# Kernel tuning notes

Measured on AMD Instinct MI355X. Metric: run time of the kernel, lower is better.

## Reference

```python
import jax, jax.numpy as jnp
import numpy as np

B, S, D, H = 32, 256, 64, 512


def setup_inputs() -> dict:
    key = jax.random.key(0)
    ks = jax.random.split(key, 8)
    s = 1.0 / np.sqrt(H)
    u = lambda k, shp: jax.random.uniform(k, shp, jnp.float32, -s, s)
    return {
        "x": jax.random.normal(ks[0], (B, S, D), jnp.float32),
        "hidden_0": jax.random.normal(ks[1], (1, B, D), jnp.float32),
        "W_hid": u(ks[2], (H, D)),
        "b_hid": u(ks[3], (H,)),
        "W_ih": u(ks[4], (4 * H, S * D)),
        "W_hh": u(ks[5], (4 * H, H)),
        "b_ih": u(ks[6], (4 * H,)),
        "b_hh": u(ks[7], (4 * H,)),
    }


def reference(x, hidden_0, W_hid, b_hid, W_ih, W_hh, b_ih, b_hh):
    b, s, d = x.shape
    # h_0 = Linear(hidden_0): [1, B, H]; used as both h and c initial state
    h0 = hidden_0 @ W_hid.T + b_hid
    # growing triangular mask [S, S] (row i has i+1 ones)
    mask = jnp.tril(jnp.ones((s, s), x.dtype))
    # [B, S, S, D] -> [B, S, S*D]; row t of the LSTM input is x[:, :t+1] zero-padded
    newX = (mask[None, :, :, None] * x[:, None, :, :]).reshape(b, s, s * d)

    def step(carry, x_t):
        h, c = carry
        gates = x_t @ W_ih.T + h @ W_hh.T + (b_ih + b_hh)  # [B, 4H]
        i, f, g, o = jnp.split(gates, 4, axis=-1)  # torch gate order i,f,g,o
        i, f, o = jax.nn.sigmoid(i), jax.nn.sigmoid(f), jax.nn.sigmoid(o)
        g = jnp.tanh(g)
        c = f * c + i * g
        h = o * jnp.tanh(c)
        return (h, c), h

    _, hs = jax.lax.scan(step, (h0[0], h0[0]), newX.transpose(1, 0, 2))
    out = jax.nn.relu(hs.transpose(1, 0, 2))  # [B, S, H]
    return out, h0
```

## Files before the change

kernel.cpp:

```cpp
#include <hip/hip_runtime.h>
#include <math.h>

typedef __attribute__((ext_vector_type(8))) short short8;
typedef __attribute__((ext_vector_type(8))) _Float16 f16x8;
typedef __attribute__((ext_vector_type(4))) float f32x4;
typedef __attribute__((ext_vector_type(4))) unsigned uint32x4;

__device__ __forceinline__ void split_f16(float f, unsigned short& h, unsigned short& l){
  _Float16 hh = (_Float16)f;
  _Float16 ll = (_Float16)(f - (float)hh);
  h = __builtin_bit_cast(unsigned short, hh);
  l = __builtin_bit_cast(unsigned short, ll);
}

__device__ __forceinline__ float fsig(float xv){ return 1.f / (1.f + __expf(-xv)); }
__device__ __forceinline__ float ftanh(float xv){ return 1.f - 2.f / (1.f + __expf(2.f * xv)); }

__global__ __launch_bounds__(256, 1) void lstm_grp(
    const float* __restrict__ x,
    const float* __restrict__ hidden0,
    const float* __restrict__ W_hid,
    const float* __restrict__ b_hid,
    const float* __restrict__ W_ih,
    const float* __restrict__ W_hh,
    const float* __restrict__ b_ih,
    const float* __restrict__ b_hh,
    float* __restrict__ out,
    float* __restrict__ out_h0,
    unsigned* __restrict__ flags,
    unsigned short* __restrict__ hloc,
    unsigned short* __restrict__ hglb,
    unsigned short* __restrict__ xhi,
    unsigned short* __restrict__ xlo)
{
  __shared__ unsigned short hsb[2][16 * 64 * 8];

  const int tid  = threadIdx.x;
  const int bid  = blockIdx.x;
  const int grp  = bid & 7;
  const int slot = bid >> 3;
  const int lane = tid & 63;
  const int wid  = tid >> 6;
  const int m    = lane & 15;
  const int g    = lane >> 4;
  const int J0   = slot * 16;
  const int gid  = bid * 256 + tid;

  const int lbm   = m & 3;
  const int b_o   = grp * 4 + lbm;
  const int j_own = J0 + wid * 4 + g;
  const int R     = (m & 3) * 512 + J0 + wid * 4 + (m >> 2);
  const bool owner = (m < 4);

  unsigned short* hlg = hloc + (size_t)grp * 256 * 2048;
  unsigned short* hgg = hglb + (size_t)grp * 256 * 2048;

  {
    const float4* x4 = (const float4*)x;
    float4 f0 = x4[(size_t)gid * 2];
    float4 f1 = x4[(size_t)gid * 2 + 1];
    float fs[8] = {f0.x,f0.y,f0.z,f0.w,f1.x,f1.y,f1.z,f1.w};
    uint32x4 hv4, lv4;
    #pragma unroll
    for (int i = 0; i < 4; ++i){
      unsigned short h0b, l0b, h1b, l1b;
      split_f16(fs[2*i],   h0b, l0b);
      split_f16(fs[2*i+1], h1b, l1b);
      hv4[i] = (unsigned)h0b | ((unsigned)h1b << 16);
      lv4[i] = (unsigned)l0b | ((unsigned)l1b << 16);
    }
    asm volatile("global_store_dwordx4 %0, %1, off sc0 sc1" :: "v"(xhi + (size_t)gid*8), "v"(hv4) : "memory");
    asm volatile("global_store_dwordx4 %0, %1, off sc0 sc1" :: "v"(xlo + (size_t)gid*8), "v"(lv4) : "memory");
  }

  float c_state;
  {
    const float* hv = hidden0 + b_o * 64;
    const float* wv = W_hid + j_own * 64;
    float acc = b_hid[j_own];
    #pragma unroll
    for (int d = 0; d < 64; d += 4){
      float4 a = *(const float4*)(hv + d);
      float4 w = *(const float4*)(wv + d);
      acc += a.x*w.x + a.y*w.y + a.z*w.z + a.w*w.w;
    }
    c_state = acc;
    if (owner){
      out_h0[(size_t)b_o * 512 + j_own] = acc;
      unsigned short hh, ll; split_f16(acc, hh, ll);
      unsigned vh = hh;
      size_t off = (size_t)lbm * 512 + j_own;
      asm volatile("global_store_short %0, %1, off"         :: "v"(hlg + off), "v"(vh) : "memory");
      asm volatile("global_store_short %0, %1, off sc0 sc1" :: "v"(hgg + off), "v"(vh) : "memory");
    }
  }

  f16x8 whh_hi[16], whh_lo[16];
  #pragma unroll
  for (int kc = 0; kc < 16; ++kc){
    const float* p = W_hh + (size_t)R * 512 + kc * 32 + g * 8;
    float4 f0 = *(const float4*)p;
    float4 f1 = *(const float4*)(p + 4);
    float fs[8] = {f0.x,f0.y,f0.z,f0.w,f1.x,f1.y,f1.z,f1.w};
    short8 hb8, lb8;
    #pragma unroll
    for (int i = 0; i < 8; ++i){
      unsigned short hh, ll; split_f16(fs[i], hh, ll);
      hb8[i] = (short)hh; lb8[i] = (short)ll;
    }
    whh_hi[kc] = __builtin_bit_cast(f16x8, hb8);
    whh_lo[kc] = __builtin_bit_cast(f16x8, lb8);
  }

  const float bias_i = b_ih[j_own]        + b_hh[j_own];
  const float bias_f = b_ih[512 + j_own]  + b_hh[512 + j_own];
  const float bias_g = b_ih[1024 + j_own] + b_hh[1024 + j_own];
  const float bias_o = b_ih[1536 + j_own] + b_hh[1536 + j_own];

  asm volatile("s_waitcnt vmcnt(0)" ::: "memory");
  __syncthreads();
  if (tid == 0){
    unsigned one = 1;
    asm volatile("global_store_dword %0, %1, off sc0 sc1" :: "v"(flags + bid), "v"(one) : "memory");
  }
  {
    const unsigned* fp = flags + lane * 4;
    while (true){
      uint32x4 fv;
      asm volatile("global_load_dwordx4 %0, %1, off sc0 sc1\n\ts_waitcnt vmcnt(0)"
                   : "=v"(fv) : "v"(fp) : "memory");
      unsigned mn0 = fv[0] < fv[1] ? fv[0] : fv[1];
      unsigned mn1 = fv[2] < fv[3] ? fv[2] : fv[3];
      unsigned mn  = mn0 < mn1 ? mn0 : mn1;
      if (__all((int)(mn >= 1u))) break;
      __builtin_amdgcn_s_sleep(1);
    }
  }

  f32x4 axc0 = {0.f,0.f,0.f,0.f}, axc1 = axc0, axc2 = axc0;

  auto cvt8 = [](float4 f0, float4 f1, f16x8& hi, f16x8& lo){
    float fs[8] = {f0.x,f0.y,f0.z,f0.w,f1.x,f1.y,f1.z,f1.w};
    short8 hb8, lb8;
    #pragma unroll
    for (int i = 0; i < 8; ++i){
      unsigned short hh, ll; split_f16(fs[i], hh, ll);
      hb8[i] = (short)hh; lb8[i] = (short)ll;
    }
    hi = __builtin_bit_cast(f16x8, hb8);
    lo = __builtin_bit_cast(f16x8, lb8);
  };

  {
    #pragma unroll
    for (int kc = 0; kc < 2; ++kc){
      const float* p = W_ih + (size_t)R * 16384 + kc * 32 + g * 8;
      f16x8 ahi, alo;
      cvt8(*(const float4*)p, *(const float4*)(p + 4), ahi, alo);
      size_t off = (size_t)b_o * 16384 + kc * 32 + g * 8;
      f16x8 bhi = __builtin_bit_cast(f16x8, *(const short8*)(xhi + off));
      f16x8 blo = __builtin_bit_cast(f16x8, *(const short8*)(xlo + off));
      axc0 = __builtin_amdgcn_mfma_f32_16x16x32_f16(ahi, bhi, axc0, 0,0,0);
      axc1 = __builtin_amdgcn_mfma_f32_16x16x32_f16(ahi, blo, axc1, 0,0,0);
      axc2 = __builtin_amdgcn_mfma_f32_16x16x32_f16(alo, bhi, axc2, 0,0,0);
    }
  }

  const int lb_st = tid >> 6;
  const int us_st = (tid & 63) ^ (lb_st & 7);
  bool use_local = true;

  for (int t = 0; t < 256; ++t){
    uint32x4 dv;
    bool got = false;

    if (use_local){
      const unsigned* p = (const unsigned*)(hlg + (size_t)t * 2048) + (size_t)tid * 4;
      int tries = 0;
      while (tries < 64){
        asm volatile("global_load_dwordx4 %0, %1, off sc0\n\ts_waitcnt vmcnt(0)"
                     : "=v"(dv) : "v"(p) : "memory");
        int bad = 0;
        #pragma unroll
        for (int q = 0; q < 4; ++q){
          unsigned w = dv[q];
          bad |= ((w & 0xFFFFu) == 0xFFFFu) | (w >= 0xFFFF0000u);
        }
        if (!__any(bad)){ got = true; break; }
        __builtin_amdgcn_s_sleep(1);
        ++tries;
      }
      if (!got) use_local = false;
    }
    if (!got){
      const unsigned* p = (const unsigned*)(hgg + (size_t)t * 2048) + (size_t)tid * 4;
      while (true){
        asm volatile("global_load_dwordx4 %0, %1, off sc0 sc1\n\ts_waitcnt vmcnt(0)"
                     : "=v"(dv) : "v"(p) : "memory");
        int bad = 0;
        #pragma unroll
        for (int q = 0; q < 4; ++q){
          unsigned w = dv[q];
          bad |= ((w & 0xFFFFu) == 0xFFFFu) | (w >= 0xFFFF0000u);
        }
        if (!__any(bad)) break;
        __builtin_amdgcn_s_sleep(1);
      }
    }

    float4 w0, w1, w2, w3;
    short8 xh0, xh1, xl0, xl1;
    if (t < 255){
      const float* p = W_ih + (size_t)R * 16384 + (size_t)(t+1) * 64 + g * 8;
      w0 = *(const float4*)p;        w1 = *(const float4*)(p + 4);
      w2 = *(const float4*)(p + 32); w3 = *(const float4*)(p + 36);
      size_t off = ((size_t)b_o * 256 + (size_t)(t+1)) * 64 + g * 8;
      xh0 = *(const short8*)(xhi + off);      xh1 = *(const short8*)(xhi + off + 32);
      xl0 = *(const short8*)(xlo + off);      xl1 = *(const short8*)(xlo + off + 32);
    }

    *(uint32x4*)(&hsb[t & 1][(size_t)(lb_st * 64 + us_st) * 8]) = dv;
    __syncthreads();

    f32x4 acc0 = {0.f,0.f,0.f,0.f}, acc2 = acc0;
    {
      const unsigned short* srcH = &hsb[t & 1][0];
      #pragma unroll
      for (int kc = 0; kc < 16; ++kc){
        int us = (kc * 4 + g) ^ (m & 7);
        f16x8 bhi = __builtin_bit_cast(f16x8, *(const short8*)(srcH + (size_t)(m * 64 + us) * 8));
        acc0 = __builtin_amdgcn_mfma_f32_16x16x32_f16(whh_hi[kc], bhi, acc0, 0,0,0);
        acc2 = __builtin_amdgcn_mfma_f32_16x16x32_f16(whh_lo[kc], bhi, acc2, 0,0,0);
      }
    }

    f32x4 pre = acc0 + acc2 + axc0 + axc1 + axc2;
    float ig = fsig(pre[0] + bias_i);
    float fg = fsig(pre[1] + bias_f);
    float gg = ftanh(pre[2] + bias_g);
    float og = fsig(pre[3] + bias_o);
    c_state = fg * c_state + ig * gg;
    float hval = og * ftanh(c_state);

    if (owner){
      if (t < 255){
        unsigned short hh, ll; split_f16(hval, hh, ll);
        unsigned vh = hh;
        size_t off = (size_t)(t+1) * 2048 + (size_t)lbm * 512 + j_own;
        asm volatile("global_store_short %0, %1, off"         :: "v"(hlg + off), "v"(vh) : "memory");
        asm volatile("global_store_short %0, %1, off sc0 sc1" :: "v"(hgg + off), "v"(vh) : "memory");
      }
      out[((size_t)b_o * 256 + t) * 512 + j_own] = fmaxf(hval, 0.f);
    }

    if (t < 255){
      f16x8 ahi0, alo0, ahi1, alo1;
      cvt8(w0, w1, ahi0, alo0);
      cvt8(w2, w3, ahi1, alo1);
      f16x8 bh0 = __builtin_bit_cast(f16x8, xh0), bl0 = __builtin_bit_cast(f16x8, xl0);
      f16x8 bh1 = __builtin_bit_cast(f16x8, xh1), bl1 = __builtin_bit_cast(f16x8, xl1);
      axc0 = __builtin_amdgcn_mfma_f32_16x16x32_f16(ahi0, bh0, axc0, 0,0,0);
      axc1 = __builtin_amdgcn_mfma_f32_16x16x32_f16(ahi0, bl0, axc1, 0,0,0);
      axc2 = __builtin_amdgcn_mfma_f32_16x16x32_f16(alo0, bh0, axc2, 0,0,0);
      axc0 = __builtin_amdgcn_mfma_f32_16x16x32_f16(ahi1, bh1, axc0, 0,0,0);
      axc1 = __builtin_amdgcn_mfma_f32_16x16x32_f16(ahi1, bl1, axc1, 0,0,0);
      axc2 = __builtin_amdgcn_mfma_f32_16x16x32_f16(alo1, bh1, axc2, 0,0,0);
    }
  }
}

extern "C" void kernel_launch(void* const* d_in, const int* in_sizes, int n_in,
                              void* d_out, int out_size, void* d_ws, size_t ws_size,
                              hipStream_t stream) {
  const float* x       = (const float*)d_in[0];
  const float* hidden0 = (const float*)d_in[1];
  const float* W_hid   = (const float*)d_in[2];
  const float* b_hid   = (const float*)d_in[3];
  const float* W_ih    = (const float*)d_in[4];
  const float* W_hh    = (const float*)d_in[5];
  const float* b_ih    = (const float*)d_in[6];
  const float* b_hh    = (const float*)d_in[7];

  float* out    = (float*)d_out;
  float* out_h0 = out + (size_t)32 * 256 * 512;

  char* ws = (char*)d_ws;
  unsigned*       flags = (unsigned*)ws;
  unsigned short* xhi   = (unsigned short*)(ws + 4096);
  unsigned short* xlo   = (unsigned short*)(ws + 4096 + (1<<20));
  unsigned short* hloc  = (unsigned short*)(ws + 4096 + (2<<20));
  unsigned short* hglb  = (unsigned short*)(ws + 4096 + (2<<20) + (8<<20));

  (void)hipMemsetAsync(ws, 0, 4096, stream);
  (void)hipMemsetAsync(hloc, 0xFF, (size_t)8 * 256 * 2048 * 2, stream);
  (void)hipMemsetAsync(hglb, 0xFF, (size_t)8 * 256 * 2048 * 2, stream);

  lstm_grp<<<256, 256, 0, stream>>>(
      x, hidden0, W_hid, b_hid, W_ih, W_hh, b_ih, b_hh,
      out, out_h0, flags, hloc, hglb, xhi, xlo);
}
```

Measured before the change: 571.2 us.

## Precompute per-timestep input projections in fp32 prologue, prefix-sum them in the recurrence

Replaces the per-step split-fp16 MFMA computation of the input contribution with a prologue where each block computes, for one timestep chunk, the fp32 dot product of the 64-wide x slice with W_ih for all 2048 gate rows and 32 batches, storing the results to a workspace buffer. The recurrent loop then loads one prefetched 4-gate vector per step and accumulates it as a running prefix sum, exploiting the triangular mask structure. This moves W_ih reads and fp16 split conversions off the serial critical path. In exchange it adds a large fp32 scalar-FMA prologue reading all of W_ih (128 MB), plus a 64 MB workspace. The prologue writes must be visible to other blocks before the loop reads them, and that ordering relies on the existing flag barrier.

```diff
diff --git a/kernel.cpp b/kernel.cpp
--- a/kernel.cpp
+++ b/kernel.cpp
@@ -28,10 +28,9 @@
     float* __restrict__ out,
     float* __restrict__ out_h0,
     unsigned* __restrict__ flags,
+    float* __restrict__ Zb,
     unsigned short* __restrict__ hloc,
-    unsigned short* __restrict__ hglb,
-    unsigned short* __restrict__ xhi,
-    unsigned short* __restrict__ xlo)
+    unsigned short* __restrict__ hglb)
 {
   __shared__ unsigned short hsb[2][16 * 64 * 8];
 
@@ -44,7 +43,6 @@
   const int m    = lane & 15;
   const int g    = lane >> 4;
   const int J0   = slot * 16;
-  const int gid  = bid * 256 + tid;
 
   const int lbm   = m & 3;
   const int b_o   = grp * 4 + lbm;
@@ -56,21 +54,37 @@
   unsigned short* hgg = hglb + (size_t)grp * 256 * 2048;
 
   {
-    const float4* x4 = (const float4*)x;
-    float4 f0 = x4[(size_t)gid * 2];
-    float4 f1 = x4[(size_t)gid * 2 + 1];
-    float fs[8] = {f0.x,f0.y,f0.z,f0.w,f1.x,f1.y,f1.z,f1.w};
-    uint32x4 hv4, lv4;
+    const int tz = bid;
+    const int zb = tid & 31;
+    const int jq = tid >> 5;
+    float xrow[64];
+    const float* xp = x + ((size_t)zb * 256 + tz) * 64;
     #pragma unroll
-    for (int i = 0; i < 4; ++i){
-      unsigned short h0b, l0b, h1b, l1b;
-      split_f16(fs[2*i],   h0b, l0b);
-      split_f16(fs[2*i+1], h1b, l1b);
-      hv4[i] = (unsigned)h0b | ((unsigned)h1b << 16);
-      lv4[i] = (unsigned)l0b | ((unsigned)l1b << 16);
-    }
-    asm volatile("global_store_dwordx4 %0, %1, off sc0 sc1" :: "v"(xhi + (size_t)gid*8), "v"(hv4) : "memory");
-    asm volatile("global_store_dwordx4 %0, %1, off sc0 sc1" :: "v"(xlo + (size_t)gid*8), "v"(lv4) : "memory");
+    for (int d4 = 0; d4 < 16; ++d4){
+      float4 f = *(const float4*)(xp + d4 * 4);
+      xrow[d4*4+0] = f.x; xrow[d4*4+1] = f.y;
+      xrow[d4*4+2] = f.z; xrow[d4*4+3] = f.w;
+    }
+    for (int jj = 0; jj < 64; ++jj){
+      int j = jq * 64 + jj;
+      uint32x4 zw;
+      #pragma unroll
+      for (int gate = 0; gate < 4; ++gate){
+        const float* wp = W_ih + (size_t)(gate * 512 + j) * 16384 + (size_t)tz * 64;
+        float s0 = 0.f, s1 = 0.f, s2 = 0.f, s3 = 0.f;
+        #pragma unroll
+        for (int d4 = 0; d4 < 16; ++d4){
+          float4 w = *(const float4*)(wp + d4 * 4);
+          s0 += w.x * xrow[d4*4+0];
+          s1 += w.y * xrow[d4*4+1];
+          s2 += w.z * xrow[d4*4+2];
+          s3 += w.w * xrow[d4*4+3];
+        }
+        zw[gate] = __builtin_bit_cast(unsigned, (s0 + s1) + (s2 + s3));
+      }
+      float* zp = Zb + ((size_t)((size_t)tz * 512 + j) * 32 + zb) * 4;
+      asm volatile("global_store_dwordx4 %0, %1, off sc0 sc1" :: "v"(zp), "v"(zw) : "memory");
+    }
   }
 
   float c_state;
@@ -137,40 +151,18 @@
     }
   }
 
-  f32x4 axc0 = {0.f,0.f,0.f,0.f}, axc1 = axc0, axc2 = axc0;
-
-  auto cvt8 = [](float4 f0, float4 f1, f16x8& hi, f16x8& lo){
-    float fs[8] = {f0.x,f0.y,f0.z,f0.w,f1.x,f1.y,f1.z,f1.w};
-    short8 hb8, lb8;
-    #pragma unroll
-    for (int i = 0; i < 8; ++i){
-      unsigned short hh, ll; split_f16(fs[i], hh, ll);
-      hb8[i] = (short)hh; lb8[i] = (short)ll;
-    }
-    hi = __builtin_bit_cast(f16x8, hb8);
-    lo = __builtin_bit_cast(f16x8, lb8);
-  };
-
-  {
-    #pragma unroll
-    for (int kc = 0; kc < 2; ++kc){
-      const float* p = W_ih + (size_t)R * 16384 + kc * 32 + g * 8;
-      f16x8 ahi, alo;
-      cvt8(*(const float4*)p, *(const float4*)(p + 4), ahi, alo);
-      size_t off = (size_t)b_o * 16384 + kc * 32 + g * 8;
-      f16x8 bhi = __builtin_bit_cast(f16x8, *(const short8*)(xhi + off));
-      f16x8 blo = __builtin_bit_cast(f16x8, *(const short8*)(xlo + off));
-      axc0 = __builtin_amdgcn_mfma_f32_16x16x32_f16(ahi, bhi, axc0, 0,0,0);
-      axc1 = __builtin_amdgcn_mfma_f32_16x16x32_f16(ahi, blo, axc1, 0,0,0);
-      axc2 = __builtin_amdgcn_mfma_f32_16x16x32_f16(alo, bhi, axc2, 0,0,0);
-    }
-  }
-
   const int lb_st = tid >> 6;
   const int us_st = (tid & 63) ^ (lb_st & 7);
   bool use_local = true;
 
+  f32x4 axc = {0.f, 0.f, 0.f, 0.f};
+  f32x4 zc = *(const f32x4*)(Zb + ((size_t)((size_t)0 * 512 + j_own) * 32 + b_o) * 4);
+
   for (int t = 0; t < 256; ++t){
+    f32x4 zn;
+    if (t < 255)
+      zn = *(const f32x4*)(Zb + ((size_t)((size_t)(t+1) * 512 + j_own) * 32 + b_o) * 4);
+
     uint32x4 dv;
     bool got = false;
 
@@ -208,17 +200,6 @@
       }
     }
 
-    float4 w0, w1, w2, w3;
-    short8 xh0, xh1, xl0, xl1;
-    if (t < 255){
-      const float* p = W_ih + (size_t)R * 16384 + (size_t)(t+1) * 64 + g * 8;
-      w0 = *(const float4*)p;        w1 = *(const float4*)(p + 4);
-      w2 = *(const float4*)(p + 32); w3 = *(const float4*)(p + 36);
-      size_t off = ((size_t)b_o * 256 + (size_t)(t+1)) * 64 + g * 8;
-      xh0 = *(const short8*)(xhi + off);      xh1 = *(const short8*)(xhi + off + 32);
-      xl0 = *(const short8*)(xlo + off);      xl1 = *(const short8*)(xlo + off + 32);
-    }
-
     *(uint32x4*)(&hsb[t & 1][(size_t)(lb_st * 64 + us_st) * 8]) = dv;
     __syncthreads();
 
@@ -234,7 +215,9 @@
       }
     }
 
-    f32x4 pre = acc0 + acc2 + axc0 + axc1 + axc2;
+    axc += zc;
+
+    f32x4 pre = acc0 + acc2 + axc;
     float ig = fsig(pre[0] + bias_i);
     float fg = fsig(pre[1] + bias_f);
     float gg = ftanh(pre[2] + bias_g);
@@ -253,19 +236,7 @@
       out[((size_t)b_o * 256 + t) * 512 + j_own] = fmaxf(hval, 0.f);
     }
 
-    if (t < 255){
-      f16x8 ahi0, alo0, ahi1, alo1;
-      cvt8(w0, w1, ahi0, alo0);
-      cvt8(w2, w3, ahi1, alo1);
-      f16x8 bh0 = __builtin_bit_cast(f16x8, xh0), bl0 = __builtin_bit_cast(f16x8, xl0);
-      f16x8 bh1 = __builtin_bit_cast(f16x8, xh1), bl1 = __builtin_bit_cast(f16x8, xl1);
-      axc0 = __builtin_amdgcn_mfma_f32_16x16x32_f16(ahi0, bh0, axc0, 0,0,0);
-      axc1 = __builtin_amdgcn_mfma_f32_16x16x32_f16(ahi0, bl0, axc1, 0,0,0);
-      axc2 = __builtin_amdgcn_mfma_f32_16x16x32_f16(alo0, bh0, axc2, 0,0,0);
-      axc0 = __builtin_amdgcn_mfma_f32_16x16x32_f16(ahi1, bh1, axc0, 0,0,0);
-      axc1 = __builtin_amdgcn_mfma_f32_16x16x32_f16(ahi1, bl1, axc1, 0,0,0);
-      axc2 = __builtin_amdgcn_mfma_f32_16x16x32_f16(alo1, bh1, axc2, 0,0,0);
-    }
+    zc = zn;
   }
 }
 
@@ -286,10 +257,9 @@
 
   char* ws = (char*)d_ws;
   unsigned*       flags = (unsigned*)ws;
-  unsigned short* xhi   = (unsigned short*)(ws + 4096);
-  unsigned short* xlo   = (unsigned short*)(ws + 4096 + (1<<20));
-  unsigned short* hloc  = (unsigned short*)(ws + 4096 + (2<<20));
-  unsigned short* hglb  = (unsigned short*)(ws + 4096 + (2<<20) + (8<<20));
+  float*          Zb    = (float*)(ws + 4096);
+  unsigned short* hloc  = (unsigned short*)(ws + 4096 + (64u<<20));
+  unsigned short* hglb  = (unsigned short*)(ws + 4096 + (72u<<20));
 
   (void)hipMemsetAsync(ws, 0, 4096, stream);
   (void)hipMemsetAsync(hloc, 0xFF, (size_t)8 * 256 * 2048 * 2, stream);
@@ -297,5 +267,5 @@
 
   lstm_grp<<<256, 256, 0, stream>>>(
       x, hidden0, W_hid, b_hid, W_ih, W_hh, b_ih, b_hh,
-      out, out_h0, flags, hloc, hglb, xhi, xlo);
+      out, out_h0, flags, Zb, hloc, hglb);
 }
```

Result: slower. 743.7 us (+30.2%).

## Pack per-step hidden state in LDS and publish with vector stores

Applied to the files above, without the earlier changes.

Each block now gathers its 64 fp16 hidden values in shared memory and 8 threads write them with 16-byte stores to both the local and global exchange buffers. Previously every owner lane issued scattered 2-byte stores. The exchange buffer layout changes from batch-major to slot-major, and the LDS scatter indexing on the read side is updated to match. The output store moves after the input MFMA prefetch. The change aims to cut the number of coherent store transactions on the critical path between steps, at the cost of one extra block barrier per step.

```diff
diff --git a/kernel.cpp b/kernel.cpp
--- a/kernel.cpp
+++ b/kernel.cpp
@@ -34,6 +34,7 @@
     unsigned short* __restrict__ xlo)
 {
   __shared__ unsigned short hsb[2][16 * 64 * 8];
+  __shared__ unsigned short hpk[64];
 
   const int tid  = threadIdx.x;
   const int bid  = blockIdx.x;
@@ -88,10 +89,7 @@
     if (owner){
       out_h0[(size_t)b_o * 512 + j_own] = acc;
       unsigned short hh, ll; split_f16(acc, hh, ll);
-      unsigned vh = hh;
-      size_t off = (size_t)lbm * 512 + j_own;
-      asm volatile("global_store_short %0, %1, off"         :: "v"(hlg + off), "v"(vh) : "memory");
-      asm volatile("global_store_short %0, %1, off sc0 sc1" :: "v"(hgg + off), "v"(vh) : "memory");
+      hpk[m * 16 + wid * 4 + g] = hh;
     }
   }
 
@@ -117,6 +115,14 @@
   const float bias_g = b_ih[1024 + j_own] + b_hh[1024 + j_own];
   const float bias_o = b_ih[1536 + j_own] + b_hh[1536 + j_own];
 
+  __syncthreads();
+  if (tid < 8){
+    uint32x4 pk = *(const uint32x4*)(hpk + tid * 8);
+    unsigned short* d0 = hlg + (size_t)slot * 64 + tid * 8;
+    unsigned short* d1 = hgg + (size_t)slot * 64 + tid * 8;
+    asm volatile("global_store_dwordx4 %0, %1, off"         :: "v"(d0), "v"(pk) : "memory");
+    asm volatile("global_store_dwordx4 %0, %1, off sc0 sc1" :: "v"(d1), "v"(pk) : "memory");
+  }
   asm volatile("s_waitcnt vmcnt(0)" ::: "memory");
   __syncthreads();
   if (tid == 0){
@@ -166,8 +172,11 @@
     }
   }
 
-  const int lb_st = tid >> 6;
-  const int us_st = (tid & 63) ^ (lb_st & 7);
+  const int sl_src = tid >> 3;
+  const int r8     = tid & 7;
+  const int lb_c   = r8 >> 1;
+  const int u_c    = sl_src * 2 + (r8 & 1);
+  const int us_c   = u_c ^ lb_c;
   bool use_local = true;
 
   for (int t = 0; t < 256; ++t){
@@ -219,7 +228,7 @@
       xl0 = *(const short8*)(xlo + off);      xl1 = *(const short8*)(xlo + off + 32);
     }
 
-    *(uint32x4*)(&hsb[t & 1][(size_t)(lb_st * 64 + us_st) * 8]) = dv;
+    *(uint32x4*)(&hsb[t & 1][(size_t)(lb_c * 64 + us_c) * 8]) = dv;
     __syncthreads();
 
     f32x4 acc0 = {0.f,0.f,0.f,0.f}, acc2 = acc0;
@@ -243,14 +252,17 @@
     float hval = og * ftanh(c_state);
 
     if (owner){
-      if (t < 255){
-        unsigned short hh, ll; split_f16(hval, hh, ll);
-        unsigned vh = hh;
-        size_t off = (size_t)(t+1) * 2048 + (size_t)lbm * 512 + j_own;
-        asm volatile("global_store_short %0, %1, off"         :: "v"(hlg + off), "v"(vh) : "memory");
-        asm volatile("global_store_short %0, %1, off sc0 sc1" :: "v"(hgg + off), "v"(vh) : "memory");
-      }
-      out[((size_t)b_o * 256 + t) * 512 + j_own] = fmaxf(hval, 0.f);
+      unsigned short hh, ll; split_f16(hval, hh, ll);
+      hpk[m * 16 + wid * 4 + g] = hh;
+    }
+    __syncthreads();
+
+    if (t < 255 && tid < 8){
+      uint32x4 pk = *(const uint32x4*)(hpk + tid * 8);
+      unsigned short* d0 = hlg + (size_t)(t+1) * 2048 + (size_t)slot * 64 + tid * 8;
+      unsigned short* d1 = hgg + (size_t)(t+1) * 2048 + (size_t)slot * 64 + tid * 8;
+      asm volatile("global_store_dwordx4 %0, %1, off"         :: "v"(d0), "v"(pk) : "memory");
+      asm volatile("global_store_dwordx4 %0, %1, off sc0 sc1" :: "v"(d1), "v"(pk) : "memory");
     }
 
     if (t < 255){
@@ -266,6 +278,9 @@
       axc1 = __builtin_amdgcn_mfma_f32_16x16x32_f16(ahi1, bl1, axc1, 0,0,0);
       axc2 = __builtin_amdgcn_mfma_f32_16x16x32_f16(alo1, bh1, axc2, 0,0,0);
     }
+
+    if (owner)
+      out[((size_t)b_o * 256 + t) * 512 + j_own] = fmaxf(hval, 0.f);
   }
 }
 
```

After: 484.1 us. -15.2%, faster.
